# Performance work log

Measured on AMD Instinct MI355X. Metric: run time of the kernel, lower is better.

Reference implementation:

```python
import jax, jax.numpy as jnp
import numpy as np
import math

EPS = 1e-8


def _l2_normalize(v, axis=-1, eps=EPS):
    # Matches torch.nn.functional.normalize: v / max(||v||, eps)
    n = jnp.sqrt(jnp.sum(v * v, axis=axis, keepdims=True))
    return v / jnp.maximum(n, eps)


def _gelu_tanh(x):
    c = math.sqrt(2.0 / math.pi)
    return 0.5 * x * (1.0 + jnp.tanh(c * (x + 0.044715 * x * x * x)))


def setup_inputs() -> dict:
    key = jax.random.key(0)
    k1, k2, k3, k4 = jax.random.split(key, 4)
    B, T, D, K = 8, 4096, 2048, 8
    x = jax.random.normal(k1, (B, T, D), dtype=jnp.float32)
    # module initializes prototypes as normalized randn(K, D)
    P = jax.random.normal(k2, (K, D), dtype=jnp.float32)
    P = _l2_normalize(P)
    log_tau = jnp.asarray(math.log(2.0), dtype=jnp.float32)
    log_blend = jnp.asarray(math.log(0.3 / 0.7), dtype=jnp.float32)
    return {"x": x, "prototypes": P, "log_tau": log_tau, "log_blend": log_blend}


def reference(x, prototypes, log_tau, log_blend):
    tau = jnp.exp(log_tau)
    alpha = jax.nn.sigmoid(log_blend)
    B, T, D = x.shape
    x_norm = _l2_normalize(x)                      # (B, T, D)
    p_norm = _l2_normalize(prototypes)             # (K, D)
    sims = jnp.einsum('btd,kd->btk', x_norm, p_norm)  # tiny K=8 matmul
    sims = jnp.clip(sims, -1.0, 1.0)
    min_dist = jnp.min(1.0 - sims, axis=-1)        # (B, T)
    min_dist = jnp.clip(min_dist, 0.0, 2.0)
    novelty = 1.0 - jnp.exp(-tau * min_dist)       # (B, T)
    scale = 1.0 - alpha + alpha * novelty[..., None]
    scale = jnp.clip(scale, 0.1, 10.0)
    return _gelu_tanh(x * scale)
```

## Files before the change

kernel.cpp:

```cpp
#include <hip/hip_runtime.h>
#include <math.h>

#define D 2048
#define K 8
#define BLOCK 512
#define RPW 4

typedef __fp16 h2 __attribute__((ext_vector_type(2)));
typedef __fp16 h4 __attribute__((ext_vector_type(4)));

__device__ __forceinline__ float rcp_fast(float x) {
    return __builtin_amdgcn_rcpf(x);
}

#if __has_builtin(__builtin_amdgcn_fdot2)
#define FDOT2(a, b, c) __builtin_amdgcn_fdot2((a), (b), (c), false)
#else
__device__ __forceinline__ float fdot2_emul(h2 a, h2 b, float c) {
    return fmaf((float)a[0], (float)b[0], fmaf((float)a[1], (float)b[1], c));
}
#define FDOT2 fdot2_emul
#endif

__device__ __forceinline__ float gelu_tanh_fast(float y) {
    const float nc = -2.3022078977f;
    float w = y * fmaf(0.044715f, y * y, 1.0f);
    return y * rcp_fast(1.0f + exp2f(nc * w));
}

__device__ __forceinline__ float dot4f(const float4& a, const float4& b) {
    return fmaf(a.w, b.w, fmaf(a.z, b.z, fmaf(a.y, b.y, a.x * b.x)));
}

#define FOLDSTEP(x, y, m)                                   \
    {                                                       \
        float _k = (lane & (m)) ? (y) : (x);                \
        float _o = (lane & (m)) ? (x) : (y);                \
        x = _k + __shfl_xor(_o, (m));                       \
    }

__global__ __launch_bounds__(BLOCK, 2)
void novelty_gelu_wave(const float* __restrict__ x,
                       const float* __restrict__ P,
                       const float* __restrict__ plog_tau,
                       const float* __restrict__ plog_blend,
                       float* __restrict__ out,
                       int nrows)
{
    __shared__ h4    pf[K * 512];
    __shared__ float s_inv[K];

    const int tid  = threadIdx.x;
    const int wave = tid >> 6;
    const int lane = tid & 63;

    {
        const float* pr = P + wave * D;
        float s = 0.f;
        #pragma unroll
        for (int j = 0; j < 8; ++j) {
            float4 p = *(const float4*)(pr + (j * 64 + lane) * 4);
            s += dot4f(p, p);
        }
        #pragma unroll
        for (int m = 1; m < 64; m <<= 1) s += __shfl_xor(s, m);
        if (lane == 0) s_inv[wave] = 1.0f / fmaxf(sqrtf(s), 1e-8f);
    }
    __syncthreads();

    #pragma unroll
    for (int k = 0; k < K; ++k) {
        const float inv = s_inv[k];
        float4 p = *(const float4*)(P + k * D + tid * 4);
        h2 lo = __builtin_amdgcn_cvt_pkrtz(p.x * inv, p.y * inv);
        h2 hi = __builtin_amdgcn_cvt_pkrtz(p.z * inv, p.w * inv);
        pf[k * 512 + tid] = __builtin_shufflevector(lo, hi, 0, 1, 2, 3);
    }
    __syncthreads();

    const float tau   = __expf(plog_tau[0]);
    const float alpha = 1.0f / (1.0f + __expf(-plog_blend[0]));
    const float oma   = 1.0f - alpha;

    const int wid = blockIdx.x * (BLOCK / 64) + wave;
    int row = wid * RPW;
    int limit = row + RPW;
    if (limit > nrows) limit = nrows;

    for (; row < limit; ++row) {
        const float* xr = x + (size_t)row * D;

        h2 xh[16];
        float ssq = 0.f;
        float dt[K];
        #pragma unroll
        for (int k = 0; k < K; ++k) dt[k] = 0.f;

        #pragma unroll
        for (int g = 0; g < 2; ++g) {
            float4 v[4];
            #pragma unroll
            for (int j = 0; j < 4; ++j)
                v[j] = *(const float4*)(xr + ((g * 4 + j) * 64 + lane) * 4);

            #pragma unroll
            for (int j = 0; j < 4; ++j) {
                const int c = g * 4 + j;
                h2 xlo = __builtin_amdgcn_cvt_pkrtz(v[j].x, v[j].y);
                h2 xhi = __builtin_amdgcn_cvt_pkrtz(v[j].z, v[j].w);
                xh[2 * c]     = xlo;
                xh[2 * c + 1] = xhi;
                ssq = FDOT2(xlo, xlo, ssq);
                ssq = FDOT2(xhi, xhi, ssq);
                #pragma unroll
                for (int k = 0; k < K; ++k) {
                    h4 p  = pf[k * 512 + c * 64 + lane];
                    h2 lo = __builtin_shufflevector(p, p, 0, 1);
                    h2 hi = __builtin_shufflevector(p, p, 2, 3);
                    dt[k] = FDOT2(xlo, lo, dt[k]);
                    dt[k] = FDOT2(xhi, hi, dt[k]);
                }
            }
        }

        FOLDSTEP(dt[0], dt[1], 1);
        FOLDSTEP(dt[2], dt[3], 1);
        FOLDSTEP(dt[4], dt[5], 1);
        FOLDSTEP(dt[6], dt[7], 1);
        FOLDSTEP(dt[0], dt[2], 2);
        FOLDSTEP(dt[4], dt[6], 2);
        FOLDSTEP(dt[0], dt[4], 4);
        float vd = dt[0];
        vd += __shfl_xor(vd, 8);
        vd += __shfl_xor(vd, 16);
        vd += __shfl_xor(vd, 32);
        float dmax = vd;
        dmax = fmaxf(dmax, __shfl_xor(dmax, 1));
        dmax = fmaxf(dmax, __shfl_xor(dmax, 2));
        dmax = fmaxf(dmax, __shfl_xor(dmax, 4));
        #pragma unroll
        for (int m = 1; m < 64; m <<= 1) ssq += __shfl_xor(ssq, m);

        const float inv_nx = 1.0f / fmaxf(sqrtf(ssq), 1e-8f);
        float sim = fminf(1.0f, fmaxf(-1.0f, dmax * inv_nx));
        float md  = fminf(fmaxf(1.0f - sim, 0.0f), 2.0f);
        float scale = oma + alpha * (1.0f - __expf(-tau * md));
        scale = fminf(fmaxf(scale, 0.1f), 10.0f);

        float* outr = out + (size_t)row * D;
        #pragma unroll
        for (int c = 0; c < 8; ++c) {
            float4 o;
            o.x = gelu_tanh_fast((float)xh[2 * c][0]     * scale);
            o.y = gelu_tanh_fast((float)xh[2 * c][1]     * scale);
            o.z = gelu_tanh_fast((float)xh[2 * c + 1][0] * scale);
            o.w = gelu_tanh_fast((float)xh[2 * c + 1][1] * scale);
            *(float4*)(outr + (c * 64 + lane) * 4) = o;
        }
    }
}

extern "C" void kernel_launch(void* const* d_in, const int* in_sizes, int n_in,
                              void* d_out, int out_size, void* d_ws, size_t ws_size,
                              hipStream_t stream) {
    const float* x  = (const float*)d_in[0];
    const float* P  = (const float*)d_in[1];
    const float* lt = (const float*)d_in[2];
    const float* lb = (const float*)d_in[3];
    float* out = (float*)d_out;

    const int nrows = in_sizes[0] / D;
    const int waves = BLOCK / 64;
    int grid = (nrows + waves * RPW - 1) / (waves * RPW);

    novelty_gelu_wave<<<grid, BLOCK, 0, stream>>>(x, P, lt, lb, out, nrows);
}
```

Measured before the change: 112.3 us.

## Split fused kernel into scale computation and separate GELU apply pass

Splits the single fused kernel into two. The first computes per-row novelty scales into workspace, and the second re-reads x in fp32 and applies scale and GELU with a grid-stride elementwise loop. This removes the register-held fp16 copy of each row and decouples the reduction phase from the store phase, so occupancy may improve. The cost is reading x a second time from memory and a second launch. It also raises accuracy, since the output now uses the original fp32 x instead of the fp16-rounded values.

```diff
diff --git a/kernel.cpp b/kernel.cpp
--- a/kernel.cpp
+++ b/kernel.cpp
@@ -40,12 +40,12 @@
     }
 
 __global__ __launch_bounds__(BLOCK, 2)
-void novelty_gelu_wave(const float* __restrict__ x,
-                       const float* __restrict__ P,
-                       const float* __restrict__ plog_tau,
-                       const float* __restrict__ plog_blend,
-                       float* __restrict__ out,
-                       int nrows)
+void scale_kernel(const float* __restrict__ x,
+                  const float* __restrict__ P,
+                  const float* __restrict__ plog_tau,
+                  const float* __restrict__ plog_blend,
+                  float* __restrict__ scales,
+                  int nrows)
 {
     __shared__ h4    pf[K * 512];
     __shared__ float s_inv[K];
@@ -90,7 +90,6 @@
     for (; row < limit; ++row) {
         const float* xr = x + (size_t)row * D;
 
-        h2 xh[16];
         float ssq = 0.f;
         float dt[K];
         #pragma unroll
@@ -108,8 +107,6 @@
                 const int c = g * 4 + j;
                 h2 xlo = __builtin_amdgcn_cvt_pkrtz(v[j].x, v[j].y);
                 h2 xhi = __builtin_amdgcn_cvt_pkrtz(v[j].z, v[j].w);
-                xh[2 * c]     = xlo;
-                xh[2 * c + 1] = xhi;
                 ssq = FDOT2(xlo, xlo, ssq);
                 ssq = FDOT2(xhi, xhi, ssq);
                 #pragma unroll
@@ -147,16 +144,27 @@
         float scale = oma + alpha * (1.0f - __expf(-tau * md));
         scale = fminf(fmaxf(scale, 0.1f), 10.0f);
 
-        float* outr = out + (size_t)row * D;
-        #pragma unroll
-        for (int c = 0; c < 8; ++c) {
-            float4 o;
-            o.x = gelu_tanh_fast((float)xh[2 * c][0]     * scale);
-            o.y = gelu_tanh_fast((float)xh[2 * c][1]     * scale);
-            o.z = gelu_tanh_fast((float)xh[2 * c + 1][0] * scale);
-            o.w = gelu_tanh_fast((float)xh[2 * c + 1][1] * scale);
-            *(float4*)(outr + (c * 64 + lane) * 4) = o;
-        }
+        if (lane == 0) scales[row] = scale;
+    }
+}
+
+__global__ __launch_bounds__(256, 8)
+void apply_kernel(const float* __restrict__ x,
+                  const float* __restrict__ scales,
+                  float* __restrict__ out,
+                  int n4)
+{
+    const int stride = gridDim.x * 256;
+    int i = blockIdx.x * 256 + threadIdx.x;
+    for (; i < n4; i += stride) {
+        float4 v = *(const float4*)(x + (size_t)i * 4);
+        const float sc = scales[i >> 9];
+        float4 o;
+        o.x = gelu_tanh_fast(v.x * sc);
+        o.y = gelu_tanh_fast(v.y * sc);
+        o.z = gelu_tanh_fast(v.z * sc);
+        o.w = gelu_tanh_fast(v.w * sc);
+        *(float4*)(out + (size_t)i * 4) = o;
     }
 }
 
@@ -167,11 +175,15 @@
     const float* P  = (const float*)d_in[1];
     const float* lt = (const float*)d_in[2];
     const float* lb = (const float*)d_in[3];
-    float* out = (float*)d_out;
+    float* out    = (float*)d_out;
+    float* scales = (float*)d_ws;
 
     const int nrows = in_sizes[0] / D;
+    const int n4    = in_sizes[0] / 4;
+
     const int waves = BLOCK / 64;
-    int grid = (nrows + waves * RPW - 1) / (waves * RPW);
+    int grid1 = (nrows + waves * RPW - 1) / (waves * RPW);
 
-    novelty_gelu_wave<<<grid, BLOCK, 0, stream>>>(x, P, lt, lb, out, nrows);
+    scale_kernel<<<grid1, BLOCK, 0, stream>>>(x, P, lt, lb, scales, nrows);
+    apply_kernel<<<2048, 256, 0, stream>>>(x, scales, out, n4);
 }
```

After: 175.3 us. 56.1% more time.
